# Performance work log

Measured on AMD Instinct MI355X. Metric: run time of the kernel, lower is better.

The kernel has to match this reference:

```python
import jax, jax.numpy as jnp
import numpy as np

IMAGE_SIZE = (1536, 1536)
STRIDE = 2
W_OUT = IMAGE_SIZE[0] // STRIDE  # 768
H_OUT = IMAGE_SIZE[1] // STRIDE  # 768
N_BOXES = 128


def setup_inputs() -> dict:
    key = jax.random.key(0)
    k1, k2, k3 = jax.random.split(key, 3)
    conf = jax.random.uniform(k1, (1, H_OUT, W_OUT), dtype=jnp.float32)
    # bboxes in xyxy format, guaranteed inside the image with positive area
    wh = jax.random.uniform(k2, (N_BOXES, 2), minval=8.0, maxval=160.0, dtype=jnp.float32)
    cxy = jax.random.uniform(k3, (N_BOXES, 2), minval=96.0, maxval=float(IMAGE_SIZE[0]) - 96.0, dtype=jnp.float32)
    bboxes = jnp.concatenate([cxy - wh / 2.0, cxy + wh / 2.0], axis=1)
    return {"conf": conf, "bboxes": bboxes}


def reference(conf, bboxes):
    # conf: [1, H, W] predicted confidence map (batch must be 1, as in the original)
    # bboxes: [N, 4] xyxy
    c = conf[0]  # [H, W]
    x1, y1, x2, y2 = bboxes[:, 0], bboxes[:, 1], bboxes[:, 2], bboxes[:, 3]
    valid = ((x2 - x1) * (y2 - y1)) > 0  # skip zero-area boxes (obj_area == 0)
    # reference-point positions: centers of stride-sized cells
    px = (jnp.arange(W_OUT, dtype=c.dtype) + 0.5) * STRIDE  # [W]
    py = (jnp.arange(H_OUT, dtype=c.dtype) + 0.5) * STRIDE  # [H]
    # point-in-bbox containment test (is_point_in_bbox): x1 <= px <= x2, y1 <= py <= y2
    inx = (px[None, :] >= x1[:, None]) & (px[None, :] <= x2[:, None])  # [N, W]
    iny = (py[None, :] >= y1[:, None]) & (py[None, :] <= y2[:, None])  # [N, H]
    contains = valid[:, None, None] & iny[:, :, None] & inx[:, None, :]  # [N, H, W]
    # ownership resolution (box_ids_map semantics):
    #   a grid point claimed by exactly one box keeps that box's id,
    #   a point claimed by >= 2 boxes is set to -1 (ambiguous), unclaimed -> -1
    count = contains.sum(axis=0)  # [H, W]
    first = jnp.argmax(contains, axis=0)  # id of first (only) claiming box
    owner = jnp.where(count == 1, first, -1)  # [H, W]
    # per-box positive_points_map and post_score = max(conf * map)
    mask = (owner[None, :, :] == jnp.arange(N_BOXES)[:, None, None]).astype(c.dtype)  # [N, H, W]
    scores = jnp.max(c[None, :, :] * mask, axis=(1, 2))  # [N]; boxes with no points get 0
    return scores
```

## Files before the change

kernel.cpp:

```cpp
#include <hip/hip_runtime.h>
#include <hip/hip_bf16.h>

#define W_OUT 768
#define H_OUT 768
#define N_BOXES 128
#define NCHUNK 16

__global__ __launch_bounds__(256) void box_chunk_kernel(
    const float* __restrict__ conf,
    const float* __restrict__ boxes,
    unsigned int* __restrict__ partial) {
    __shared__ float4 ovl[N_BOXES];
    __shared__ float wred[4];

    const int tid = threadIdx.x;
    const int lane = tid & 63;
    const int ty = tid >> 6;
    const int b = blockIdx.x >> 4;
    const int chunk = blockIdx.x & (NCHUNK - 1);

    const float4* b4 = (const float4*)boxes;
    const float4 me = b4[b];
    if ((me.z - me.x) * (me.w - me.y) <= 0.0f) {
        if (tid == 0) partial[blockIdx.x] = 0u;
        return;
    }

    const float4 ba = b4[lane];
    const float4 bb = b4[64 + lane];
    const bool ia = (ba.z - ba.x) * (ba.w - ba.y) > 0.0f &&
                    ba.x <= me.z && ba.z >= me.x && ba.y <= me.w && ba.w >= me.y;
    const bool ib = (bb.z - bb.x) * (bb.w - bb.y) > 0.0f &&
                    bb.x <= me.z && bb.z >= me.x && bb.y <= me.w && bb.w >= me.y;
    unsigned long long m0 = __ballot(ia);
    unsigned long long m1 = __ballot(ib);
    if (b < 64) m0 &= ~(1ull << b);
    else        m1 &= ~(1ull << (b - 64));
    const int n0 = __popcll(m0);
    const int novl = n0 + __popcll(m1);

    if (tid < 64) {
        if (m0 & (1ull << lane))
            ovl[__popcll(m0 & ((1ull << lane) - 1))] = ba;
        if (m1 & (1ull << lane))
            ovl[n0 + __popcll(m1 & ((1ull << lane) - 1))] = bb;
    }
    __syncthreads();

    const int x0 = max(0, (int)floorf(me.x * 0.5f - 0.5f) - 1);
    const int x1 = min(W_OUT - 1, (int)ceilf(me.z * 0.5f) + 1);
    const int y0 = max(0, (int)floorf(me.y * 0.5f - 0.5f) - 1);
    const int y1 = min(H_OUT - 1, (int)ceilf(me.w * 0.5f) + 1);
    const int per = ((y1 - y0 + 1) + NCHUNK - 1) >> 4;
    const int yc0 = y0 + chunk * per;
    const int yc1 = min(y1, yc0 + per - 1);

    float lmax = 0.0f;
    for (int yy = yc0 + ty; yy <= yc1; yy += 4) {
        const float py = (yy + 0.5f) * 2.0f;
        if (py < me.y || py > me.w) continue;
        for (int xx = x0 + lane; xx <= x1; xx += 64) {
            const float px = (xx + 0.5f) * 2.0f;
            if (px < me.x || px > me.z) continue;
            bool excl = true;
            for (int k = 0; k < novl; ++k) {
                const float4 o = ovl[k];
                if (px >= o.x && px <= o.z && py >= o.y && py <= o.w) {
                    excl = false;
                    break;
                }
            }
            if (excl) lmax = fmaxf(lmax, conf[yy * W_OUT + xx]);
        }
    }

    for (int off = 32; off > 0; off >>= 1)
        lmax = fmaxf(lmax, __shfl_xor(lmax, off));
    if (lane == 0) wred[ty] = lmax;
    __syncthreads();
    if (tid == 0) {
        const float v = fmaxf(fmaxf(wred[0], wred[1]), fmaxf(wred[2], wred[3]));
        partial[blockIdx.x] = __float_as_uint(v);
    }
}

__global__ __launch_bounds__(256) void reduce_kernel(
    const unsigned int* __restrict__ partial,
    float* __restrict__ scores) {
    const int t = threadIdx.x;
    const uint4* p4 = (const uint4*)partial;

    const uint4 a = p4[t];
    const uint4 c = p4[t + 256];
    unsigned int v1 = max(max(a.x, a.y), max(a.z, a.w));
    unsigned int v2 = max(max(c.x, c.y), max(c.z, c.w));
#pragma unroll
    for (int off = 1; off <= 2; off <<= 1) {
        const unsigned int o1 = (unsigned int)__shfl_xor((int)v1, off);
        const unsigned int o2 = (unsigned int)__shfl_xor((int)v2, off);
        v1 = v1 > o1 ? v1 : o1;
        v2 = v2 > o2 ? v2 : o2;
    }
    if ((t & 3) == 0) {
        scores[t >> 2] = __uint_as_float(v1);
        scores[64 + (t >> 2)] = __uint_as_float(v2);
    }
}

extern "C" void kernel_launch(void* const* d_in, const int* in_sizes, int n_in,
                              void* d_out, int out_size, void* d_ws, size_t ws_size,
                              hipStream_t stream) {
    const float* conf = (const float*)d_in[0];
    const float* boxes = (const float*)d_in[1];
    float* scores = (float*)d_out;
    unsigned int* partial = (unsigned int*)d_ws;

    box_chunk_kernel<<<N_BOXES * NCHUNK, 256, 0, stream>>>(conf, boxes, partial);
    reduce_kernel<<<1, 256, 0, stream>>>(partial, scores);
}
```

Before: 14.18 us.

## Use one 1024-thread block per box and drop the separate reduce kernel

Replaces the 16-chunk-per-box grid of 256-thread blocks plus a second reduction launch with a single launch of 128 blocks of 1024 threads. Each block covers its whole box and reduces the maximum in shared memory, removing the partial buffer and one kernel launch. The first four overlap boxes are also cached in registers with an unrolled branchless test. The cost is fewer, larger blocks (128 on a GPU with many CUs), so per-box work imbalance and occupancy could hurt.

```diff
diff --git a/kernel.cpp b/kernel.cpp
--- a/kernel.cpp
+++ b/kernel.cpp
@@ -4,25 +4,23 @@
 #define W_OUT 768
 #define H_OUT 768
 #define N_BOXES 128
-#define NCHUNK 16
 
-__global__ __launch_bounds__(256) void box_chunk_kernel(
+__global__ __launch_bounds__(1024) void box_kernel(
     const float* __restrict__ conf,
     const float* __restrict__ boxes,
-    unsigned int* __restrict__ partial) {
+    float* __restrict__ scores) {
     __shared__ float4 ovl[N_BOXES];
-    __shared__ float wred[4];
+    __shared__ float wred[16];
 
     const int tid = threadIdx.x;
     const int lane = tid & 63;
-    const int ty = tid >> 6;
-    const int b = blockIdx.x >> 4;
-    const int chunk = blockIdx.x & (NCHUNK - 1);
+    const int wv = tid >> 6;
+    const int b = blockIdx.x;
 
     const float4* b4 = (const float4*)boxes;
     const float4 me = b4[b];
     if ((me.z - me.x) * (me.w - me.y) <= 0.0f) {
-        if (tid == 0) partial[blockIdx.x] = 0u;
+        if (tid == 0) scores[b] = 0.0f;
         return;
     }
 
@@ -47,63 +45,50 @@
     }
     __syncthreads();
 
+    float4 oreg[4];
+#pragma unroll
+    for (int k = 0; k < 4; ++k) {
+        if (k < novl) oreg[k] = ovl[k];
+        else          oreg[k] = make_float4(3e30f, 3e30f, -3e30f, -3e30f);
+    }
+
     const int x0 = max(0, (int)floorf(me.x * 0.5f - 0.5f) - 1);
     const int x1 = min(W_OUT - 1, (int)ceilf(me.z * 0.5f) + 1);
     const int y0 = max(0, (int)floorf(me.y * 0.5f - 0.5f) - 1);
     const int y1 = min(H_OUT - 1, (int)ceilf(me.w * 0.5f) + 1);
-    const int per = ((y1 - y0 + 1) + NCHUNK - 1) >> 4;
-    const int yc0 = y0 + chunk * per;
-    const int yc1 = min(y1, yc0 + per - 1);
 
     float lmax = 0.0f;
-    for (int yy = yc0 + ty; yy <= yc1; yy += 4) {
+    for (int yy = y0 + wv; yy <= y1; yy += 16) {
         const float py = (yy + 0.5f) * 2.0f;
-        if (py < me.y || py > me.w) continue;
+        const bool rowin = (py >= me.y) && (py <= me.w);
         for (int xx = x0 + lane; xx <= x1; xx += 64) {
             const float px = (xx + 0.5f) * 2.0f;
-            if (px < me.x || px > me.z) continue;
-            bool excl = true;
-            for (int k = 0; k < novl; ++k) {
-                const float4 o = ovl[k];
-                if (px >= o.x && px <= o.z && py >= o.y && py <= o.w) {
-                    excl = false;
-                    break;
+            if (!rowin || px < me.x || px > me.z) continue;
+            bool hit = false;
+#pragma unroll
+            for (int k = 0; k < 4; ++k)
+                hit |= (px >= oreg[k].x) && (px <= oreg[k].z) &&
+                       (py >= oreg[k].y) && (py <= oreg[k].w);
+            if (!hit && novl > 4) {
+                for (int k = 4; k < novl && !hit; ++k) {
+                    const float4 o = ovl[k];
+                    hit = (px >= o.x) && (px <= o.z) &&
+                          (py >= o.y) && (py <= o.w);
                 }
             }
-            if (excl) lmax = fmaxf(lmax, conf[yy * W_OUT + xx]);
+            if (!hit) lmax = fmaxf(lmax, conf[yy * W_OUT + xx]);
         }
     }
 
     for (int off = 32; off > 0; off >>= 1)
         lmax = fmaxf(lmax, __shfl_xor(lmax, off));
-    if (lane == 0) wred[ty] = lmax;
+    if (lane == 0) wred[wv] = lmax;
     __syncthreads();
-    if (tid == 0) {
-        const float v = fmaxf(fmaxf(wred[0], wred[1]), fmaxf(wred[2], wred[3]));
-        partial[blockIdx.x] = __float_as_uint(v);
-    }
-}
-
-__global__ __launch_bounds__(256) void reduce_kernel(
-    const unsigned int* __restrict__ partial,
-    float* __restrict__ scores) {
-    const int t = threadIdx.x;
-    const uint4* p4 = (const uint4*)partial;
-
-    const uint4 a = p4[t];
-    const uint4 c = p4[t + 256];
-    unsigned int v1 = max(max(a.x, a.y), max(a.z, a.w));
-    unsigned int v2 = max(max(c.x, c.y), max(c.z, c.w));
-#pragma unroll
-    for (int off = 1; off <= 2; off <<= 1) {
-        const unsigned int o1 = (unsigned int)__shfl_xor((int)v1, off);
-        const unsigned int o2 = (unsigned int)__shfl_xor((int)v2, off);
-        v1 = v1 > o1 ? v1 : o1;
-        v2 = v2 > o2 ? v2 : o2;
-    }
-    if ((t & 3) == 0) {
-        scores[t >> 2] = __uint_as_float(v1);
-        scores[64 + (t >> 2)] = __uint_as_float(v2);
+    if (tid < 64) {
+        float v = (lane < 16) ? wred[lane] : 0.0f;
+        for (int off = 8; off > 0; off >>= 1)
+            v = fmaxf(v, __shfl_xor(v, off));
+        if (lane == 0) scores[b] = v;
     }
 }
 
@@ -113,8 +98,6 @@
     const float* conf = (const float*)d_in[0];
     const float* boxes = (const float*)d_in[1];
     float* scores = (float*)d_out;
-    unsigned int* partial = (unsigned int*)d_ws;
 
-    box_chunk_kernel<<<N_BOXES * NCHUNK, 256, 0, stream>>>(conf, boxes, partial);
-    reduce_kernel<<<1, 256, 0, stream>>>(partial, scores);
+    box_kernel<<<N_BOXES, 1024, 0, stream>>>(conf, boxes, scores);
 }
```

Result: faster. 13.68 us (-3.5%).
